# Kernel optimization log

Measured on AMD Instinct MI355X. Metric: run time of the kernel, lower is better.

Reference implementation:

```python
import jax, jax.numpy as jnp
import numpy as np

N_NODES = 50000
N_EDGES = 800000
D_IN = 256
D_HID = 128


def setup_inputs() -> dict:
    key = jax.random.key(0)
    ks = jax.random.split(key, 10)
    x = jax.random.normal(ks[0], (N_NODES, D_IN), dtype=jnp.float32)
    edge_index = jax.random.randint(ks[1], (2, N_EDGES), 0, N_NODES, dtype=jnp.int64)
    # GCNConv params (glorot-ish init), 3 layers: 256->128, 128->128, 128->128
    def glorot(k, fan_in, fan_out):
        s = jnp.sqrt(6.0 / (fan_in + fan_out))
        return jax.random.uniform(k, (fan_in, fan_out), jnp.float32, -s, s)
    W0 = glorot(ks[2], D_IN, D_HID)
    b0 = jnp.zeros((D_HID,), jnp.float32)
    W1 = glorot(ks[3], D_HID, D_HID)
    b1 = jnp.zeros((D_HID,), jnp.float32)
    W2 = glorot(ks[4], D_HID, D_HID)
    b2 = jnp.zeros((D_HID,), jnp.float32)
    return {"x": x, "edge_index": edge_index, "W0": W0, "b0": b0,
            "W1": W1, "b1": b1, "W2": W2, "b2": b2}


def _gcn_conv(x, W, b, src, dst, deg_inv_sqrt, deg_inv):
    # PyG GCNConv: x' = D^{-1/2} (A + I) D^{-1/2} (x W) + b
    h = x @ W  # [N, d_out]
    norm = deg_inv_sqrt[src] * deg_inv_sqrt[dst]  # [E]
    msg = h[src] * norm[:, None]  # gather + scale, [E, d_out]
    agg = jax.ops.segment_sum(msg, dst, num_segments=x.shape[0])
    # self-loop contribution: norm = deg^{-1/2} * deg^{-1/2} = 1/deg
    return agg + h * deg_inv[:, None] + b


def reference(x, edge_index, W0, b0, W1, b1, W2, b2):
    src, dst = edge_index[0], edge_index[1]
    n = x.shape[0]
    # degree with self loops (computed on destination, source_to_target flow)
    deg = jax.ops.segment_sum(jnp.ones((src.shape[0],), x.dtype), dst,
                              num_segments=n) + 1.0
    deg_inv_sqrt = deg ** -0.5
    deg_inv = 1.0 / deg
    h = jax.nn.relu(_gcn_conv(x, W0, b0, src, dst, deg_inv_sqrt, deg_inv))
    h = jax.nn.relu(_gcn_conv(h, W1, b1, src, dst, deg_inv_sqrt, deg_inv))
    h = jax.nn.relu(_gcn_conv(h, W2, b2, src, dst, deg_inv_sqrt, deg_inv))
    return h
```

## Files before the change

kernel.cpp:

```cpp
#include <hip/hip_runtime.h>

#define N_NODES 50000
#define N_EDGES 800000
#define D_HID   128

typedef unsigned int uint;
typedef unsigned short ushort;
typedef __attribute__((ext_vector_type(8))) short short8;
typedef __attribute__((ext_vector_type(4))) float f32x4;

#define SCAN_NB ((N_NODES + 255) / 256)
#define NB       196
#define CAP      6144
#define P1_BLOCKS 200
#define P1_CHUNK  4000

__global__ __launch_bounds__(256) void part_k(const int* __restrict__ src,
                                              const int* __restrict__ dst,
                                              int* __restrict__ bcur,
                                              int2* __restrict__ ebuf, int e) {
    __shared__ int hist[NB];
    __shared__ int base[NB];
    int tid = threadIdx.x;
    if (tid < NB) hist[tid] = 0;
    __syncthreads();

    int e0 = blockIdx.x * P1_CHUNK;
    int2 ed[16];
    bool val[16];
#pragma unroll
    for (int i = 0; i < 16; ++i) {
        int o = i * 256 + tid;
        int idx = e0 + o;
        val[i] = (o < P1_CHUNK) && (idx < e);
        if (val[i]) {
            ed[i] = make_int2(src[idx], dst[idx]);
            atomicAdd(&hist[ed[i].y >> 8], 1);
        }
    }
    __syncthreads();
    if (tid < NB && hist[tid] > 0) base[tid] = atomicAdd(&bcur[tid], hist[tid]);
    __syncthreads();
    if (tid < NB) hist[tid] = 0;
    __syncthreads();
#pragma unroll
    for (int i = 0; i < 16; ++i) {
        if (val[i]) {
            int bk = ed[i].y >> 8;
            int o  = base[bk] + atomicAdd(&hist[bk], 1);
            if (o < CAP) ebuf[(size_t)bk * CAP + o] = ed[i];
        }
    }
}

__global__ __launch_bounds__(256) void bucket_cnt_k(const int2* __restrict__ ebuf,
                                                    const int* __restrict__ bcnt,
                                                    int* __restrict__ cnt, int n) {
    __shared__ int c[256];
    int b = blockIdx.x, tid = threadIdx.x;
    c[tid] = 0;
    __syncthreads();
    int m = bcnt[b]; if (m > CAP) m = CAP;
    for (int i = tid; i < m; i += 256)
        atomicAdd(&c[ebuf[(size_t)b * CAP + i].y & 255], 1);
    __syncthreads();
    int node = b * 256 + tid;
    if (node < n) cnt[node] = c[tid];
}

__global__ void bsum_k(const int* __restrict__ cnt, int* __restrict__ bsum, int n) {
    int i = blockIdx.x * 256 + threadIdx.x;
    int v = (i < n) ? cnt[i] : 0;
#pragma unroll
    for (int off = 32; off; off >>= 1) v += __shfl_down(v, off, 64);
    __shared__ int ws[4];
    int lane = threadIdx.x & 63, w = threadIdx.x >> 6;
    if (lane == 0) ws[w] = v;
    __syncthreads();
    if (threadIdx.x == 0) bsum[blockIdx.x] = ws[0] + ws[1] + ws[2] + ws[3];
}

__global__ void bscan_k(const int* __restrict__ bsum, int* __restrict__ boff,
                        int* __restrict__ row_ptr_end, int nb) {
    __shared__ int s[256];
    int t = threadIdx.x;
    int v = (t < nb) ? bsum[t] : 0;
    s[t] = v;
    __syncthreads();
    for (int off = 1; off < 256; off <<= 1) {
        int u = (t >= off) ? s[t - off] : 0;
        __syncthreads();
        s[t] += u;
        __syncthreads();
    }
    if (t < nb) boff[t] = s[t] - v;
    if (t == 255) *row_ptr_end = s[255];
}

__global__ void scan3_k(const int* __restrict__ cnt, const int* __restrict__ boff,
                        int* __restrict__ row_ptr, float* __restrict__ dis, int n) {
    __shared__ int s[256];
    int i = blockIdx.x * 256 + threadIdx.x;
    int t = threadIdx.x;
    int v = (i < n) ? cnt[i] : 0;
    s[t] = v;
    __syncthreads();
    for (int off = 1; off < 256; off <<= 1) {
        int u = (t >= off) ? s[t - off] : 0;
        __syncthreads();
        s[t] += u;
        __syncthreads();
    }
    if (i < n) {
        row_ptr[i] = boff[blockIdx.x] + s[t] - v;
        dis[i] = rsqrtf((float)v + 1.0f);
    }
}

__global__ __launch_bounds__(256) void csr_k(const int2* __restrict__ ebuf,
                                             const int* __restrict__ bcnt,
                                             const int* __restrict__ row_ptr,
                                             int* __restrict__ col, int n) {
    __shared__ int rp_l[257];
    __shared__ int cur[256];
    __shared__ int win[CAP];
    int b = blockIdx.x, tid = threadIdx.x;
    int node0 = b * 256;
    for (int i = tid; i < 257; i += 256) {
        int nd = node0 + i; if (nd > n) nd = n;
        rp_l[i] = row_ptr[nd];
    }
    cur[tid] = 0;
    __syncthreads();
    int base0 = rp_l[0];
    int m = bcnt[b]; if (m > CAP) m = CAP;

    for (int i = tid; i < m; i += 256) {
        int2 ed = ebuf[(size_t)b * CAP + i];
        int ll = ed.y & 255;
        int pos = rp_l[ll] + atomicAdd(&cur[ll], 1) - base0;
        win[pos] = ed.x;
    }
    __syncthreads();
    for (int i = tid; i < m; i += 256) col[base0 + i] = win[i];
}

__global__ __launch_bounds__(256) void rowsort_k(const int* __restrict__ rp,
                                                 int* __restrict__ col, int n) {
    int node = blockIdx.x * 4 + (threadIdx.x >> 6);
    if (node >= n) return;
    int lane = threadIdx.x & 63;
    int beg = rp[node], end = rp[node + 1];
    int len = end - beg;
    if (len <= 1) return;
    if (len <= 64) {
        int v = (lane < len) ? col[beg + lane] : 0x7fffffff;
#pragma unroll
        for (int k = 2; k <= 64; k <<= 1)
#pragma unroll
            for (int j = k >> 1; j > 0; j >>= 1) {
                int other = __shfl_xor(v, j);
                bool up    = (lane & k) == 0;
                bool small = (lane & j) == 0;
                v = (small == up) ? min(v, other) : max(v, other);
            }
        if (lane < len) col[beg + lane] = v;
    } else if (lane == 0) {
        for (int i = beg + 1; i < end; ++i) {
            int key = col[i]; int j = i - 1;
            while (j >= beg && col[j] > key) { col[j + 1] = col[j]; --j; }
            col[j + 1] = key;
        }
    }
}

__device__ inline ushort f2bf(float f) {
    unsigned u = __float_as_uint(f);
    unsigned rounding = 0x7fffu + ((u >> 16) & 1u);
    return (ushort)((u + rounding) >> 16);
}
__device__ inline float bf_lo(uint v) { return __uint_as_float(v << 16); }
__device__ inline float bf_hi(uint v) { return __uint_as_float(v & 0xffff0000u); }
__device__ inline short8 cvt8(float4 f0, float4 f1) {
    short8 r;
    r[0] = (short)f2bf(f0.x); r[1] = (short)f2bf(f0.y);
    r[2] = (short)f2bf(f0.z); r[3] = (short)f2bf(f0.w);
    r[4] = (short)f2bf(f1.x); r[5] = (short)f2bf(f1.y);
    r[6] = (short)f2bf(f1.z); r[7] = (short)f2bf(f1.w);
    return r;
}

__global__ void wtrans_all_k(const float* __restrict__ W0, const float* __restrict__ W1,
                             const float* __restrict__ W2, ushort* __restrict__ Wt0,
                             ushort* __restrict__ Wt1, ushort* __restrict__ Wt2,
                             uint* __restrict__ hb_padrow) {
    int i = blockIdx.x * 256 + threadIdx.x;
    if (i < 64) hb_padrow[i] = 0;
    const float* W; ushort* Wt; int K, j;
    if (i < 32768)      { W = W0; Wt = Wt0; K = 256; j = i; }
    else if (i < 49152) { W = W1; Wt = Wt1; K = 128; j = i - 32768; }
    else                { W = W2; Wt = Wt2; K = 128; j = i - 49152; }
    int k = j >> 7, n = j & 127;
    Wt[(size_t)n * K + k] = f2bf(W[j]);
}

template<int K, bool AF32>
__global__ __launch_bounds__(256) void gemm_lds_k(const void* __restrict__ Ap,
                                                  const ushort* __restrict__ Bt,
                                                  const float* __restrict__ dis,
                                                  ushort* __restrict__ H,
                                                  int M) {
    constexpr int T  = K / 32;
    constexpr int EB = AF32 ? 4 : 2;
    constexpr int RS = K * EB;
    constexpr int NL = (64 * RS) / 4096;
    __shared__ char As[64 * RS];

    int tid = threadIdx.x;
    int w = tid >> 6, l = tid & 63, lr = l & 15, hi = l >> 4;
    int cBase = w * 32;

    short8 b[2][T];
#pragma unroll
    for (int c = 0; c < 2; ++c)
#pragma unroll
        for (int t = 0; t < T; ++t)
            b[c][t] = *(const short8*)&Bt[(size_t)(cBase + c * 16 + lr) * K + t * 32 + hi * 8];

    int r0 = blockIdx.x * 64;
    const char* gbase = (const char*)Ap + (size_t)r0 * RS;

#pragma unroll
    for (int i = 0; i < NL; ++i) {
        int L   = i * 4096 + tid * 16;
        int row = L / RS;
        int cb  = (L % RS) >> 4;
        const char* srcp = (r0 + row < M) ? (gbase + (size_t)row * RS + ((size_t)cb << 4))
                                          : gbase;
        uint4 v = *(const uint4*)srcp;
        *(uint4*)&As[row * RS + ((cb ^ (row & 7)) << 4)] = v;
    }
    __syncthreads();

    f32x4 acc[4][2];
#pragma unroll
    for (int rb = 0; rb < 4; ++rb)
#pragma unroll
        for (int c = 0; c < 2; ++c) acc[rb][c] = (f32x4){0.f, 0.f, 0.f, 0.f};

#pragma unroll
    for (int rb = 0; rb < 4; ++rb) {
        int row = rb * 16 + lr;
        int s = row & 7;
        const char* rbase = &As[row * RS];
#pragma unroll
        for (int t = 0; t < T; ++t) {
            short8 a;
            if constexpr (AF32) {
                int cb0 = t * 8 + hi * 2;
                float4 f0 = *(const float4*)(rbase + ((cb0 ^ s) << 4));
                float4 f1 = *(const float4*)(rbase + (((cb0 + 1) ^ s) << 4));
                a = cvt8(f0, f1);
            } else {
                int cb0 = t * 4 + hi;
                a = *(const short8*)(rbase + ((cb0 ^ s) << 4));
            }
#pragma unroll
            for (int c = 0; c < 2; ++c)
                acc[rb][c] = __builtin_amdgcn_mfma_f32_16x16x32_bf16(a, b[c][t], acc[rb][c], 0, 0, 0);
        }
    }

#pragma unroll
    for (int rb = 0; rb < 4; ++rb) {
#pragma unroll
        for (int j = 0; j < 4; ++j) {
            int r = r0 + rb * 16 + hi * 4 + j;
            if (r < M) {
                float d = dis[r];
#pragma unroll
                for (int c = 0; c < 2; ++c)
                    H[(size_t)r * 128 + cBase + c * 16 + lr] = f2bf(acc[rb][c][j] * d);
            }
        }
    }
}

template<bool LAST>
__global__ __launch_bounds__(256) void aggregate_k(const ushort* __restrict__ hs,
                                                   const int* __restrict__ row_ptr,
                                                   const int* __restrict__ col,
                                                   const float* __restrict__ dis,
                                                   const float* __restrict__ bias,
                                                   ushort* __restrict__ act,
                                                   float* __restrict__ out, int n) {
    int node = blockIdx.x * 4 + (threadIdx.x >> 6);
    if (node >= n) return;
    int lane = threadIdx.x & 63;
    int g  = lane >> 4;
    int cl = lane & 15;
    const char* base = (const char*)hs + (cl << 4);

    float ax[8];
#pragma unroll
    for (int j = 0; j < 8; ++j) ax[j] = 0.f;

    int beg = row_ptr[node], end = row_ptr[node + 1];
    for (int e = beg; e < end; e += 32) {
        int s[8];
#pragma unroll
        for (int q = 0; q < 8; ++q) {
            int idx = e + q * 4 + g;
            s[q] = (idx < end) ? col[idx] : N_NODES;
        }
        uint4 u[8];
#pragma unroll
        for (int q = 0; q < 8; ++q)
            u[q] = *(const uint4*)(base + ((size_t)s[q] << 8));
#pragma unroll
        for (int q = 0; q < 8; ++q) {
            ax[0] += bf_lo(u[q].x); ax[1] += bf_hi(u[q].x);
            ax[2] += bf_lo(u[q].y); ax[3] += bf_hi(u[q].y);
            ax[4] += bf_lo(u[q].z); ax[5] += bf_hi(u[q].z);
            ax[6] += bf_lo(u[q].w); ax[7] += bf_hi(u[q].w);
        }
    }
#pragma unroll
    for (int j = 0; j < 8; ++j) {
        ax[j] += __shfl_xor(ax[j], 16);
        ax[j] += __shfl_xor(ax[j], 32);
    }
    if (g == 0) {
        float dn = dis[node];
        uint4 un = *(const uint4*)(base + ((size_t)node << 8));
        float hsn[8] = {bf_lo(un.x), bf_hi(un.x), bf_lo(un.y), bf_hi(un.y),
                        bf_lo(un.z), bf_hi(un.z), bf_lo(un.w), bf_hi(un.w)};
        int c0 = cl * 8;
        float4 bv0 = *(const float4*)&bias[c0];
        float4 bv1 = *(const float4*)&bias[c0 + 4];
        float bb[8] = {bv0.x, bv0.y, bv0.z, bv0.w, bv1.x, bv1.y, bv1.z, bv1.w};
        float o[8];
#pragma unroll
        for (int j = 0; j < 8; ++j)
            o[j] = fmaxf((ax[j] + hsn[j]) * dn + bb[j], 0.f);
        if (LAST) {
            *(float4*)&out[(size_t)node * D_HID + c0]     = make_float4(o[0], o[1], o[2], o[3]);
            *(float4*)&out[(size_t)node * D_HID + c0 + 4] = make_float4(o[4], o[5], o[6], o[7]);
        } else {
            uint4 p;
            p.x = (uint)f2bf(o[0]) | ((uint)f2bf(o[1]) << 16);
            p.y = (uint)f2bf(o[2]) | ((uint)f2bf(o[3]) << 16);
            p.z = (uint)f2bf(o[4]) | ((uint)f2bf(o[5]) << 16);
            p.w = (uint)f2bf(o[6]) | ((uint)f2bf(o[7]) << 16);
            *(uint4*)((char*)act + ((size_t)node << 8) + (cl << 4)) = p;
        }
    }
}

extern "C" void kernel_launch(void* const* d_in, const int* in_sizes, int n_in,
                              void* d_out, int out_size, void* d_ws, size_t ws_size,
                              hipStream_t stream) {
    const float* x  = (const float*)d_in[0];
    const int*   ei = (const int*)d_in[1];
    const float* W0 = (const float*)d_in[2];
    const float* b0 = (const float*)d_in[3];
    const float* W1 = (const float*)d_in[4];
    const float* b1 = (const float*)d_in[5];
    const float* W2 = (const float*)d_in[6];
    const float* b2 = (const float*)d_in[7];
    float* out = (float*)d_out;

    const int N = N_NODES, E = N_EDGES;
    const int* src = ei;
    const int* dst = ei + E;

    char* w = (char*)d_ws;
    size_t off = 0;
    auto alloc = [&](size_t bytes) {
        size_t o = off;
        off += (bytes + 255) & ~(size_t)255;
        return o;
    };
    int*    cnt    = (int*)(w + alloc((size_t)N * 4));
    int*    bcur   = (int*)(w + alloc((size_t)NB * 4));
    float*  dis    = (float*)(w + alloc((size_t)N * 4));
    int*    rp     = (int*)(w + alloc((size_t)(N + 1) * 4));
    int*    bsum   = (int*)(w + alloc((size_t)SCAN_NB * 4));
    int*    boff   = (int*)(w + alloc((size_t)SCAN_NB * 4));
    int*    col    = (int*)(w + alloc((size_t)E * 4));
    int2*   ebuf   = (int2*)(w + alloc((size_t)NB * CAP * 8));
    ushort* hb     = (ushort*)(w + alloc((size_t)(N + 1) * D_HID * 2));
    ushort* act    = (ushort*)(w + alloc((size_t)N * D_HID * 2));
    ushort* Wt0    = (ushort*)(w + alloc((size_t)128 * 256 * 2));
    ushort* Wt1    = (ushort*)(w + alloc((size_t)128 * 128 * 2));
    ushort* Wt2    = (ushort*)(w + alloc((size_t)128 * 128 * 2));
    (void)ws_size; (void)n_in; (void)in_sizes; (void)out_size;

    hipMemsetAsync(bcur, 0, (size_t)NB * 4, stream);

    part_k<<<P1_BLOCKS, 256, 0, stream>>>(src, dst, bcur, ebuf, E);
    bucket_cnt_k<<<NB, 256, 0, stream>>>(ebuf, bcur, cnt, N);
    bsum_k<<<SCAN_NB, 256, 0, stream>>>(cnt, bsum, N);
    bscan_k<<<1, 256, 0, stream>>>(bsum, boff, rp + N, SCAN_NB);
    scan3_k<<<SCAN_NB, 256, 0, stream>>>(cnt, boff, rp, dis, N);
    csr_k<<<NB, 256, 0, stream>>>(ebuf, bcur, rp, col, N);
    rowsort_k<<<(N + 3) / 4, 256, 0, stream>>>(rp, col, N);

    wtrans_all_k<<<256, 256, 0, stream>>>(W0, W1, W2, Wt0, Wt1, Wt2,
                                          (uint*)(hb + (size_t)N * D_HID));

    int nt64 = (N + 63) / 64;
    int agg_grid = (N + 3) / 4;

    gemm_lds_k<256, true><<<nt64, 256, 0, stream>>>(x, Wt0, dis, hb, N);
    aggregate_k<false><<<agg_grid, 256, 0, stream>>>(hb, rp, col, dis, b0, act, out, N);
    gemm_lds_k<128, false><<<nt64, 256, 0, stream>>>(act, Wt1, dis, hb, N);
    aggregate_k<false><<<agg_grid, 256, 0, stream>>>(hb, rp, col, dis, b1, act, out, N);
    gemm_lds_k<128, false><<<nt64, 256, 0, stream>>>(act, Wt2, dis, hb, N);
    aggregate_k<true><<<agg_grid, 256, 0, stream>>>(hb, rp, col, dis, b2, act, out, N);
}
```

Before: 232.3 us.

## Fuse CSR count/scan kernels, use direct global-to-LDS loads, prescale column offsets

Merges the per-node counting and scanning kernels into one kernel per 256-node bucket, which takes its offset from a single scan over the bucket counts, so two launches and the cnt/bsum buffers go away. The GEMM now stages A through global_load_lds straight into LDS with the swizzle applied on the source address, and the first layer uses 32-row tiles to get more blocks. Column indices are stored pre-shifted as byte offsets, which removes a shift from every neighbour gather in aggregation. The risks are an int overflow in the shifted index (it stays within range here) and the lower per-block work in the first GEMM.

```diff
diff --git a/kernel.cpp b/kernel.cpp
--- a/kernel.cpp
+++ b/kernel.cpp
@@ -9,7 +9,6 @@
 typedef __attribute__((ext_vector_type(8))) short short8;
 typedef __attribute__((ext_vector_type(4))) float f32x4;
 
-#define SCAN_NB ((N_NODES + 255) / 256)
 #define NB       196
 #define CAP      6144
 #define P1_BLOCKS 200
@@ -53,38 +52,11 @@
     }
 }
 
-__global__ __launch_bounds__(256) void bucket_cnt_k(const int2* __restrict__ ebuf,
-                                                    const int* __restrict__ bcnt,
-                                                    int* __restrict__ cnt, int n) {
-    __shared__ int c[256];
-    int b = blockIdx.x, tid = threadIdx.x;
-    c[tid] = 0;
-    __syncthreads();
-    int m = bcnt[b]; if (m > CAP) m = CAP;
-    for (int i = tid; i < m; i += 256)
-        atomicAdd(&c[ebuf[(size_t)b * CAP + i].y & 255], 1);
-    __syncthreads();
-    int node = b * 256 + tid;
-    if (node < n) cnt[node] = c[tid];
-}
-
-__global__ void bsum_k(const int* __restrict__ cnt, int* __restrict__ bsum, int n) {
-    int i = blockIdx.x * 256 + threadIdx.x;
-    int v = (i < n) ? cnt[i] : 0;
-#pragma unroll
-    for (int off = 32; off; off >>= 1) v += __shfl_down(v, off, 64);
-    __shared__ int ws[4];
-    int lane = threadIdx.x & 63, w = threadIdx.x >> 6;
-    if (lane == 0) ws[w] = v;
-    __syncthreads();
-    if (threadIdx.x == 0) bsum[blockIdx.x] = ws[0] + ws[1] + ws[2] + ws[3];
-}
-
-__global__ void bscan_k(const int* __restrict__ bsum, int* __restrict__ boff,
-                        int* __restrict__ row_ptr_end, int nb) {
+__global__ void bscan196_k(const int* __restrict__ bcur, int* __restrict__ boff,
+                           int* __restrict__ row_ptr_end) {
     __shared__ int s[256];
     int t = threadIdx.x;
-    int v = (t < nb) ? bsum[t] : 0;
+    int v = (t < NB) ? bcur[t] : 0;
     s[t] = v;
     __syncthreads();
     for (int off = 1; off < 256; off <<= 1) {
@@ -93,27 +65,37 @@
         s[t] += u;
         __syncthreads();
     }
-    if (t < nb) boff[t] = s[t] - v;
+    if (t < NB) boff[t] = s[t] - v;
     if (t == 255) *row_ptr_end = s[255];
 }
 
-__global__ void scan3_k(const int* __restrict__ cnt, const int* __restrict__ boff,
-                        int* __restrict__ row_ptr, float* __restrict__ dis, int n) {
+__global__ __launch_bounds__(256) void cntscan_k(const int2* __restrict__ ebuf,
+                                                 const int* __restrict__ bcnt,
+                                                 const int* __restrict__ boff,
+                                                 int* __restrict__ row_ptr,
+                                                 float* __restrict__ dis, int n) {
+    __shared__ int c[256];
     __shared__ int s[256];
-    int i = blockIdx.x * 256 + threadIdx.x;
-    int t = threadIdx.x;
-    int v = (i < n) ? cnt[i] : 0;
-    s[t] = v;
+    int b = blockIdx.x, tid = threadIdx.x;
+    c[tid] = 0;
+    __syncthreads();
+    int m = bcnt[b]; if (m > CAP) m = CAP;
+    for (int i = tid; i < m; i += 256)
+        atomicAdd(&c[ebuf[(size_t)b * CAP + i].y & 255], 1);
+    __syncthreads();
+    int v = c[tid];
+    s[tid] = v;
     __syncthreads();
     for (int off = 1; off < 256; off <<= 1) {
-        int u = (t >= off) ? s[t - off] : 0;
+        int u = (tid >= off) ? s[tid - off] : 0;
         __syncthreads();
-        s[t] += u;
+        s[tid] += u;
         __syncthreads();
     }
-    if (i < n) {
-        row_ptr[i] = boff[blockIdx.x] + s[t] - v;
-        dis[i] = rsqrtf((float)v + 1.0f);
+    int node = b * 256 + tid;
+    if (node < n) {
+        row_ptr[node] = boff[b] + s[tid] - v;
+        dis[node] = rsqrtf((float)v + 1.0f);
     }
 }
 
@@ -139,7 +121,7 @@
         int2 ed = ebuf[(size_t)b * CAP + i];
         int ll = ed.y & 255;
         int pos = rp_l[ll] + atomicAdd(&cur[ll], 1) - base0;
-        win[pos] = ed.x;
+        win[pos] = ed.x << 8;
     }
     __syncthreads();
     for (int i = tid; i < m; i += 256) col[base0 + i] = win[i];
@@ -190,6 +172,12 @@
     return r;
 }
 
+__device__ inline void gload16(const void* g, void* l) {
+    __builtin_amdgcn_global_load_lds(
+        (const __attribute__((address_space(1))) uint*)g,
+        (__attribute__((address_space(3))) uint*)l, 16, 0, 0);
+}
+
 __global__ void wtrans_all_k(const float* __restrict__ W0, const float* __restrict__ W1,
                              const float* __restrict__ W2, ushort* __restrict__ Wt0,
                              ushort* __restrict__ Wt1, ushort* __restrict__ Wt2,
@@ -204,7 +192,7 @@
     Wt[(size_t)n * K + k] = f2bf(W[j]);
 }
 
-template<int K, bool AF32>
+template<int K, int ROWS, bool AF32>
 __global__ __launch_bounds__(256) void gemm_lds_k(const void* __restrict__ Ap,
                                                   const ushort* __restrict__ Bt,
                                                   const float* __restrict__ dis,
@@ -213,8 +201,8 @@
     constexpr int T  = K / 32;
     constexpr int EB = AF32 ? 4 : 2;
     constexpr int RS = K * EB;
-    constexpr int NL = (64 * RS) / 4096;
-    __shared__ char As[64 * RS];
+    constexpr int NI = (ROWS * RS) / 4096;
+    __shared__ char As[ROWS * RS];
 
     int tid = threadIdx.x;
     int w = tid >> 6, l = tid & 63, lr = l & 15, hi = l >> 4;
@@ -227,29 +215,29 @@
         for (int t = 0; t < T; ++t)
             b[c][t] = *(const short8*)&Bt[(size_t)(cBase + c * 16 + lr) * K + t * 32 + hi * 8];
 
-    int r0 = blockIdx.x * 64;
+    int r0 = blockIdx.x * ROWS;
     const char* gbase = (const char*)Ap + (size_t)r0 * RS;
 
 #pragma unroll
-    for (int i = 0; i < NL; ++i) {
-        int L   = i * 4096 + tid * 16;
+    for (int i = 0; i < NI; ++i) {
+        int L0  = (i * 4 + w) * 1024;
+        int L   = L0 + l * 16;
         int row = L / RS;
         int cb  = (L % RS) >> 4;
-        const char* srcp = (r0 + row < M) ? (gbase + (size_t)row * RS + ((size_t)cb << 4))
-                                          : gbase;
-        uint4 v = *(const uint4*)srcp;
-        *(uint4*)&As[row * RS + ((cb ^ (row & 7)) << 4)] = v;
-    }
-    __syncthreads();
-
-    f32x4 acc[4][2];
-#pragma unroll
-    for (int rb = 0; rb < 4; ++rb)
+        int gb  = (cb ^ (row & 7)) << 4;
+        int grow = (r0 + row < M) ? row : 0;
+        gload16(gbase + (size_t)grow * RS + gb, &As[L0]);
+    }
+    __syncthreads();
+
+    f32x4 acc[ROWS / 16][2];
+#pragma unroll
+    for (int rb = 0; rb < ROWS / 16; ++rb)
 #pragma unroll
         for (int c = 0; c < 2; ++c) acc[rb][c] = (f32x4){0.f, 0.f, 0.f, 0.f};
 
 #pragma unroll
-    for (int rb = 0; rb < 4; ++rb) {
+    for (int rb = 0; rb < ROWS / 16; ++rb) {
         int row = rb * 16 + lr;
         int s = row & 7;
         const char* rbase = &As[row * RS];
@@ -272,7 +260,7 @@
     }
 
 #pragma unroll
-    for (int rb = 0; rb < 4; ++rb) {
+    for (int rb = 0; rb < ROWS / 16; ++rb) {
 #pragma unroll
         for (int j = 0; j < 4; ++j) {
             int r = r0 + rb * 16 + hi * 4 + j;
@@ -311,12 +299,12 @@
 #pragma unroll
         for (int q = 0; q < 8; ++q) {
             int idx = e + q * 4 + g;
-            s[q] = (idx < end) ? col[idx] : N_NODES;
+            s[q] = (idx < end) ? col[idx] : (N_NODES << 8);
         }
         uint4 u[8];
 #pragma unroll
         for (int q = 0; q < 8; ++q)
-            u[q] = *(const uint4*)(base + ((size_t)s[q] << 8));
+            u[q] = *(const uint4*)(base + (size_t)(uint)s[q]);
 #pragma unroll
         for (int q = 0; q < 8; ++q) {
             ax[0] += bf_lo(u[q].x); ax[1] += bf_hi(u[q].x);
@@ -381,12 +369,10 @@
         off += (bytes + 255) & ~(size_t)255;
         return o;
     };
-    int*    cnt    = (int*)(w + alloc((size_t)N * 4));
     int*    bcur   = (int*)(w + alloc((size_t)NB * 4));
     float*  dis    = (float*)(w + alloc((size_t)N * 4));
     int*    rp     = (int*)(w + alloc((size_t)(N + 1) * 4));
-    int*    bsum   = (int*)(w + alloc((size_t)SCAN_NB * 4));
-    int*    boff   = (int*)(w + alloc((size_t)SCAN_NB * 4));
+    int*    boff   = (int*)(w + alloc((size_t)NB * 4));
     int*    col    = (int*)(w + alloc((size_t)E * 4));
     int2*   ebuf   = (int2*)(w + alloc((size_t)NB * CAP * 8));
     ushort* hb     = (ushort*)(w + alloc((size_t)(N + 1) * D_HID * 2));
@@ -399,23 +385,22 @@
     hipMemsetAsync(bcur, 0, (size_t)NB * 4, stream);
 
     part_k<<<P1_BLOCKS, 256, 0, stream>>>(src, dst, bcur, ebuf, E);
-    bucket_cnt_k<<<NB, 256, 0, stream>>>(ebuf, bcur, cnt, N);
-    bsum_k<<<SCAN_NB, 256, 0, stream>>>(cnt, bsum, N);
-    bscan_k<<<1, 256, 0, stream>>>(bsum, boff, rp + N, SCAN_NB);
-    scan3_k<<<SCAN_NB, 256, 0, stream>>>(cnt, boff, rp, dis, N);
+    bscan196_k<<<1, 256, 0, stream>>>(bcur, boff, rp + N);
+    cntscan_k<<<NB, 256, 0, stream>>>(ebuf, bcur, boff, rp, dis, N);
     csr_k<<<NB, 256, 0, stream>>>(ebuf, bcur, rp, col, N);
     rowsort_k<<<(N + 3) / 4, 256, 0, stream>>>(rp, col, N);
 
     wtrans_all_k<<<256, 256, 0, stream>>>(W0, W1, W2, Wt0, Wt1, Wt2,
                                           (uint*)(hb + (size_t)N * D_HID));
 
-    int nt64 = (N + 63) / 64;
+    int g32 = (N + 31) / 32;
+    int g64 = (N + 63) / 64;
     int agg_grid = (N + 3) / 4;
 
-    gemm_lds_k<256, true><<<nt64, 256, 0, stream>>>(x, Wt0, dis, hb, N);
+    gemm_lds_k<256, 32, true><<<g32, 256, 0, stream>>>(x, Wt0, dis, hb, N);
     aggregate_k<false><<<agg_grid, 256, 0, stream>>>(hb, rp, col, dis, b0, act, out, N);
-    gemm_lds_k<128, false><<<nt64, 256, 0, stream>>>(act, Wt1, dis, hb, N);
+    gemm_lds_k<128, 64, false><<<g64, 256, 0, stream>>>(act, Wt1, dis, hb, N);
     aggregate_k<false><<<agg_grid, 256, 0, stream>>>(hb, rp, col, dis, b1, act, out, N);
-    gemm_lds_k<128, false><<<nt64, 256, 0, stream>>>(act, Wt2, dis, hb, N);
+    gemm_lds_k<128, 64, false><<<g64, 256, 0, stream>>>(act, Wt2, dis, hb, N);
     aggregate_k<true><<<agg_grid, 256, 0, stream>>>(hb, rp, col, dis, b2, act, out, N);
 }
```

New measurement: 230.2 us, median of 2. About the same (-0.9%).
